# Kernel optimization log

Hardware: AMD Instinct MI355X
Metric: run time of the kernel (lower is better)

Reference implementation:

```python
import jax, jax.numpy as jnp
from jax import lax
import numpy as np

# ---- module hyperparameters (from init_kwargs) ----
DIM = 256
DIM_HEAD = 64
HEADS = 4
GROUPS = 4                      # offset_groups (defaults to heads)
INNER = DIM_HEAD * HEADS        # 256
OFF_DIMS = INNER // GROUPS      # 64
DOWN = 4
KS = 6
PAD = (KS - DOWN) // 2          # 1
OFFSET_SCALE = float(DOWN)      # offset_scale defaults to down_sample_factor
CPB_DIM = DIM // 4              # 64
SCALE = DIM_HEAD ** -0.5


def make_grid(h, w, dtype):
    # torch.meshgrid(arange(w), arange(h), indexing='xy') stacked at dim 0:
    # channel 0 = x (column index), channel 1 = y (row index); shape [2,h,w]
    yy, xx = jnp.meshgrid(jnp.arange(h), jnp.arange(w), indexing='ij')
    return jnp.stack([xx, yy], axis=0).astype(dtype)


def normalize_grid_c(vg):
    # vg: [..., 2, h, w] -> [..., h, w, 2]; faithful to source: channel 0
    # normalized by (h-1), channel 1 by (w-1) (source's h/w naming quirk).
    h, w = vg.shape[-2:]
    gh = 2.0 * vg[..., 0, :, :] / max(h - 1, 1) - 1.0
    gw = 2.0 * vg[..., 1, :, :] / max(w - 1, 1) - 1.0
    return jnp.stack([gh, gw], axis=-1)


def grid_sample_zeros(img, grid):
    # F.grid_sample bilinear, padding_mode='zeros', align_corners=False
    # img: [N,C,H,W]; grid: [N,Hg,Wg,2] with (..,0)=x, (..,1)=y in [-1,1]
    N, C, H, W = img.shape
    ix = ((grid[..., 0] + 1.0) * W - 1.0) * 0.5
    iy = ((grid[..., 1] + 1.0) * H - 1.0) * 0.5
    x0 = jnp.floor(ix)
    y0 = jnp.floor(iy)

    def gather(yy, xx):
        valid = (xx >= 0) & (xx <= W - 1) & (yy >= 0) & (yy <= H - 1)
        xc = jnp.clip(xx, 0, W - 1).astype(jnp.int32)
        yc = jnp.clip(yy, 0, H - 1).astype(jnp.int32)
        vals = jax.vmap(lambda im, y_, x_: im[:, y_, x_])(img, yc, xc)  # [N,C,Hg,Wg]
        return vals * valid[:, None, :, :].astype(img.dtype)

    wa = (x0 + 1 - ix) * (y0 + 1 - iy)
    wb = (ix - x0) * (y0 + 1 - iy)
    wc = (x0 + 1 - ix) * (iy - y0)
    wd = (ix - x0) * (iy - y0)
    return (gather(y0, x0) * wa[:, None]
            + gather(y0, x0 + 1) * wb[:, None]
            + gather(y0 + 1, x0) * wc[:, None]
            + gather(y0 + 1, x0 + 1) * wd[:, None])


def gconv1x1(t, w):
    # grouped 1x1 conv (no bias): t [b, G*Ci, h, w], w [G, Co, Ci]
    G, Co, Ci = w.shape
    bb, _, hh, ww = t.shape
    tg = t.reshape(bb, G, Ci, hh, ww)
    return jnp.einsum('bgihw,goi->bgohw', tg, w).reshape(bb, G * Co, hh, ww)


def setup_inputs() -> dict:
    key = jax.random.key(0)
    ks = jax.random.split(key, 12)
    s = 0.02
    B, H, W = 8, 32, 32
    cg = DIM // GROUPS  # per-group in-channels = 64
    og = INNER // GROUPS  # per-group out-channels = 64
    return {
        'x': jax.random.normal(ks[0], (B, DIM, H, W), jnp.float32),
        'wq': jax.random.normal(ks[1], (GROUPS, og, cg), jnp.float32) * s,
        'wk': jax.random.normal(ks[2], (GROUPS, og, cg), jnp.float32) * s,
        'wv': jax.random.normal(ks[3], (GROUPS, og, cg), jnp.float32) * s,
        'w_off_dw': jax.random.normal(ks[4], (OFF_DIMS, 1, KS, KS), jnp.float32) * s,
        'b_off_dw': jnp.zeros((OFF_DIMS,), jnp.float32),
        'w_off_pw': jax.random.normal(ks[5], (2, OFF_DIMS), jnp.float32) * s,
        'cpb_w1': jax.random.normal(ks[6], (CPB_DIM, 2), jnp.float32) * s,
        'cpb_b1': jnp.zeros((CPB_DIM,), jnp.float32),
        'cpb_w2': jax.random.normal(ks[7], (CPB_DIM, CPB_DIM), jnp.float32) * s,
        'cpb_b2': jnp.zeros((CPB_DIM,), jnp.float32),
        'cpb_w3': jax.random.normal(ks[8], (HEADS // GROUPS, CPB_DIM), jnp.float32) * s,
        'cpb_b3': jnp.zeros((HEADS // GROUPS,), jnp.float32),
        'w_out': jax.random.normal(ks[9], (DIM, INNER), jnp.float32) * s,
        'b_out': jnp.zeros((DIM,), jnp.float32),
    }


def reference(x, wq, wk, wv, w_off_dw, b_off_dw, w_off_pw,
              cpb_w1, cpb_b1, cpb_w2, cpb_b2, cpb_w3, cpb_b3,
              w_out, b_out):
    b, _, H, W = x.shape

    q = gconv1x1(x, wq)                                       # [b, INNER, H, W]
    gq = q.reshape(b * GROUPS, OFF_DIMS, H, W)                # grouped queries
    gx = x.reshape(b * GROUPS, DIM // GROUPS, H, W)           # grouped input

    # to_offsets: depthwise conv -> GELU -> 1x1 conv -> tanh -> scale
    off = lax.conv_general_dilated(
        gq, w_off_dw, window_strides=(DOWN, DOWN),
        padding=[(PAD, PAD), (PAD, PAD)],
        dimension_numbers=('NCHW', 'OIHW', 'NCHW'),
        feature_group_count=OFF_DIMS)
    off = off + b_off_dw[None, :, None, None]
    off = jax.nn.gelu(off, approximate=False)
    off = jnp.einsum('bchw,oc->bohw', off, w_off_pw)
    off = jnp.tanh(off) * OFFSET_SCALE                        # [bg, 2, h2, w2]

    h2, w2 = off.shape[-2:]
    vg = make_grid(h2, w2, off.dtype)[None] + off             # [bg, 2, h2, w2]
    vgs = normalize_grid_c(vg)                                # [bg, h2, w2, 2]

    kv = grid_sample_zeros(gx, vgs)                           # [bg, DIM/G, h2, w2]
    kv = kv.reshape(b, DIM, h2, w2)
    k = gconv1x1(kv, wk)
    v = gconv1x1(kv, wv)
    q = q * SCALE

    def to_heads(t):
        bb, _, hh, ww = t.shape
        return t.reshape(bb, HEADS, DIM_HEAD, hh * ww).transpose(0, 1, 3, 2)

    qh, kh, vh = to_heads(q), to_heads(k), to_heads(v)        # [b, h, i|j, d]
    sim = jnp.einsum('bhid,bhjd->bhij', qh, kh)               # [b, h, HW, h2*w2]

    # CPB relative position bias
    grid_q = normalize_grid_c(make_grid(H, W, x.dtype)).reshape(1, H * W, 2)
    grid_kv = vgs.reshape(b * GROUPS, h2 * w2, 2)
    pos = grid_q[:, :, None, :] - grid_kv[:, None, :, :]      # [bg, i, j, 2]
    bias = jnp.sign(pos) * jnp.log1p(jnp.abs(pos))
    bias = jax.nn.relu(bias @ cpb_w1.T + cpb_b1)
    bias = jax.nn.relu(bias @ cpb_w2.T + cpb_b2)
    bias = bias @ cpb_w3.T + cpb_b3                           # [bg, i, j, o]
    o = HEADS // GROUPS
    bias = bias.reshape(b, GROUPS, H * W, h2 * w2, o)
    bias = bias.transpose(0, 1, 4, 2, 3).reshape(b, HEADS, H * W, h2 * w2)

    attn = jax.nn.softmax(sim + bias, axis=-1)
    out = jnp.einsum('bhij,bhjd->bhid', attn, vh)             # [b, h, HW, d]
    out = out.transpose(0, 1, 3, 2).reshape(b, INNER, H, W)
    out = jnp.einsum('bchw,oc->bohw', out, w_out) + b_out[None, :, None, None]
    return out
```

## Files before the change

kernel.cpp:

```cpp
#include <hip/hip_runtime.h>
#include <hip/hip_bf16.h>
#include <math.h>

#define QSCALE 0.125f

typedef __attribute__((ext_vector_type(8))) short short8b;
typedef __attribute__((ext_vector_type(8))) _Float16 half8;
typedef __attribute__((ext_vector_type(2))) _Float16 half2v;
typedef __attribute__((ext_vector_type(4))) float f32x4;

__device__ __forceinline__ uint pack2(float a, float b) {
    uint r;
    asm("v_cvt_pk_bf16_f32 %0, %1, %2" : "=v"(r) : "v"(a), "v"(b));
    return r;
}
__device__ __forceinline__ uint pkrtz(float a, float b) {
    uint r;
    asm("v_cvt_pkrtz_f16_f32 %0, %1, %2" : "=v"(r) : "v"(a), "v"(b));
    return r;
}
__device__ __forceinline__ half2v h2(uint u) { return __builtin_bit_cast(half2v, u); }
__device__ __forceinline__ float slogf_(float p) {
    return copysignf(log1pf(fabsf(p)), p);
}

__global__ __launch_bounds__(256) void k_qproj(const float* __restrict__ x,
                                               const float* __restrict__ wq,
                                               float* __restrict__ q,
                                               short* __restrict__ qbt) {
    __shared__ float Wst[64 * 68];
    __shared__ float xs[64 * 68];
    int ht = blockIdx.x, g = blockIdx.y, b = blockIdx.z;
    int tid = threadIdx.x;
    for (int e = tid; e < 4096; e += 256) {
        int co = e >> 6, ci = e & 63;
        Wst[ci * 68 + co] = wq[(g * 64 + co) * 64 + ci];
    }
    const float* xb = x + (b * 256 + g * 64) * 1024 + ht * 64;
    for (int e = tid; e < 1024; e += 256) {
        int ci = e >> 4, hq = e & 15;
        *(float4*)&xs[ci * 68 + hq * 4] = *(const float4*)&xb[ci * 1024 + hq * 4];
    }
    __syncthreads();
    int cg = tid >> 4, hg = tid & 15;
    int co0 = cg * 4, hw0 = hg * 4;
    float acc[4][4] = {};
    for (int ci = 0; ci < 64; ci++) {
        float4 a4 = *(float4*)&Wst[ci * 68 + co0];
        float4 b4 = *(float4*)&xs[ci * 68 + hw0];
        float av[4] = {a4.x, a4.y, a4.z, a4.w};
        float bv[4] = {b4.x, b4.y, b4.z, b4.w};
        #pragma unroll
        for (int a = 0; a < 4; a++)
            #pragma unroll
            for (int c = 0; c < 4; c++) acc[a][c] += av[a] * bv[c];
    }
    float* qb = q + (b * 256 + g * 64) * 1024 + ht * 64;
    for (int a = 0; a < 4; a++) {
        float4 o = {acc[a][0], acc[a][1], acc[a][2], acc[a][3]};
        *(float4*)&qb[(co0 + a) * 1024 + hw0] = o;
    }
    short* q16 = qbt + ((size_t)((b * 4 + g) * 1024 + ht * 64)) * 64;
    for (int c = 0; c < 4; c++) {
        uint2 uu;
        uu.x = pack2(acc[0][c] * QSCALE, acc[1][c] * QSCALE);
        uu.y = pack2(acc[2][c] * QSCALE, acc[3][c] * QSCALE);
        *(uint2*)&q16[(hw0 + c) * 64 + co0] = uu;
    }
}

__global__ __launch_bounds__(256) void k_dw(const float* __restrict__ q,
                                            const float* __restrict__ wdw,
                                            const float* __restrict__ bdw,
                                            float* __restrict__ gdw) {
    __shared__ float qs[8 * 1024];
    __shared__ float wds[8 * 36];
    int cg = blockIdx.x, n = blockIdx.y;
    int b = n >> 2, gg = n & 3;
    int c0 = cg * 8;
    int tid = threadIdx.x;
    const float* qn = q + (b * 256 + gg * 64 + c0) * 1024;
    for (int e = tid; e < 2048; e += 256)
        ((float4*)qs)[e] = ((const float4*)qn)[e];
    for (int e = tid; e < 288; e += 256)
        wds[e] = wdw[c0 * 36 + e];
    __syncthreads();
    for (int e = tid; e < 512; e += 256) {
        int c = e >> 6, pos = e & 63;
        int oy = pos >> 3, ox = pos & 7;
        float acc = bdw[c0 + c];
        #pragma unroll
        for (int ky = 0; ky < 6; ky++) {
            int iy = oy * 4 - 1 + ky;
            if (iy < 0 || iy > 31) continue;
            #pragma unroll
            for (int kx = 0; kx < 6; kx++) {
                int ix = ox * 4 - 1 + kx;
                if (ix < 0 || ix > 31) continue;
                acc += qs[c * 1024 + iy * 32 + ix] * wds[c * 36 + ky * 6 + kx];
            }
        }
        gdw[(n * 64 + c0 + c) * 64 + pos] = acc * 0.5f * (1.f + erff(acc * 0.70710678118654752f));
    }
}

__global__ __launch_bounds__(256) void k_pre(const float* __restrict__ x,
                                             const float* __restrict__ gdw,
                                             const float* __restrict__ wpw,
                                             const float* __restrict__ wk,
                                             const float* __restrict__ wv,
                                             const float* __restrict__ wout,
                                             const float* __restrict__ w2,
                                             float* __restrict__ vgs,
                                             uint* __restrict__ u0g,
                                             short* __restrict__ kob,
                                             short* __restrict__ vob,
                                             short* __restrict__ wob,
                                             uint* __restrict__ w2h) {
    __shared__ float gstage[4096];
    __shared__ float kvsT[64 * 68];
    __shared__ uint wkh[64 * 36];
    __shared__ uint wvh[64 * 36];
    __shared__ uint kvh[64 * 36];
    __shared__ float vx_s[64], vy_s[64];
    int n = blockIdx.x, tid = threadIdx.x;
    int b = n >> 2, g = n & 3;

    {
        int e = n * 2048 + tid * 8;
        float4 f0 = *(const float4*)&wout[e];
        float4 f1 = *(const float4*)&wout[e + 4];
        uint4 u = {pack2(f0.x, f0.y), pack2(f0.z, f0.w), pack2(f1.x, f1.y), pack2(f1.z, f1.w)};
        *(uint4*)&wob[e] = u;
    }
    if (tid < 128) {
        int idx = n * 128 + tid;
        int c2 = idx >> 5, p = idx & 31;
        float2 wv2 = *(const float2*)&w2[c2 * 64 + 2 * p];
        w2h[c2 * 32 + p] = pkrtz(wv2.x, wv2.y);
    }
    for (int e = tid; e < 2048; e += 256) {
        int co = e >> 5, p = e & 31;
        float2 a = *(const float2*)&wk[(g * 64 + co) * 64 + 2 * p];
        float2 c = *(const float2*)&wv[(g * 64 + co) * 64 + 2 * p];
        wkh[co * 36 + p] = pkrtz(a.x, a.y);
        wvh[co * 36 + p] = pkrtz(c.x, c.y);
    }
    for (int e = tid; e < 1024; e += 256)
        ((float4*)gstage)[e] = ((const float4*)(gdw + n * 4096))[e];
    __syncthreads();
    if (tid < 128) {
        int o = tid >> 6, pos = tid & 63;
        float a = 0.f;
        #pragma unroll 8
        for (int c = 0; c < 64; c++) a += gstage[c * 64 + pos] * wpw[o * 64 + c];
        float off = tanhf(a) * 4.0f;
        if (o == 0) {
            int ox = pos & 7;
            float v = 2.f * ((float)ox + off) / 7.f - 1.f;
            vx_s[pos] = v;
            vgs[(n * 64 + pos) * 2] = v;
        } else {
            int oy = pos >> 3;
            float v = 2.f * ((float)oy + off) / 7.f - 1.f;
            vy_s[pos] = v;
            vgs[(n * 64 + pos) * 2 + 1] = v;
        }
    }
    __syncthreads();
    for (int e = tid; e < 2048; e += 256) {
        int ix = e >> 6, j = e & 63;
        float qx = (2.f / 31.f) * (float)ix - 1.f;
        float u = slogf_(qx - vx_s[j]);
        u0g[n * 2048 + e] = pkrtz(u, u);
    }
    for (int e = tid; e < 4096; e += 256) {
        int c = e >> 6, pos = e & 63;
        float ix = (vx_s[pos] + 1.f) * 16.f - 0.5f;
        float iy = (vy_s[pos] + 1.f) * 16.f - 0.5f;
        float x0 = floorf(ix), y0 = floorf(iy);
        float wa = (x0 + 1.f - ix) * (y0 + 1.f - iy);
        float wb = (ix - x0) * (y0 + 1.f - iy);
        float wc = (x0 + 1.f - ix) * (iy - y0);
        float wd = (ix - x0) * (iy - y0);
        const float* img = x + (b * 256 + g * 64 + c) * 1024;
        int xi = (int)x0, yi = (int)y0;
        float acc = 0.f;
        if (xi >= 0 && xi <= 31 && yi >= 0 && yi <= 31)             acc += img[yi * 32 + xi] * wa;
        if (xi + 1 >= 0 && xi + 1 <= 31 && yi >= 0 && yi <= 31)     acc += img[yi * 32 + xi + 1] * wb;
        if (xi >= 0 && xi <= 31 && yi + 1 >= 0 && yi + 1 <= 31)     acc += img[(yi + 1) * 32 + xi] * wc;
        if (xi + 1 >= 0 && xi + 1 <= 31 && yi + 1 >= 0 && yi + 1 <= 31) acc += img[(yi + 1) * 32 + xi + 1] * wd;
        kvsT[pos * 68 + c] = acc;
    }
    __syncthreads();
    for (int e = tid; e < 2048; e += 256) {
        int pos = e >> 5, p = e & 31;
        float2 v2 = *(const float2*)&kvsT[pos * 68 + 2 * p];
        kvh[pos * 36 + p] = pkrtz(v2.x, v2.y);
    }
    __syncthreads();
    int wid = tid >> 6, lane = tid & 63, lr = lane & 15, gq = lane >> 4;
    int mat = wid >> 1, cb = (wid & 1) * 32;
    const uint* wh = mat ? wvh : wkh;
    #pragma unroll
    for (int ct2 = 0; ct2 < 2; ct2++) {
        int ct = cb + ct2 * 16;
        half8 af[2];
        #pragma unroll
        for (int s = 0; s < 2; s++)
            af[s] = __builtin_bit_cast(half8, *(const uint4*)&wh[(ct + lr) * 36 + s * 16 + gq * 4]);
        #pragma unroll
        for (int nt = 0; nt < 4; nt++) {
            half8 bf[2];
            #pragma unroll
            for (int s = 0; s < 2; s++)
                bf[s] = __builtin_bit_cast(half8, *(const uint4*)&kvh[(nt * 16 + lr) * 36 + s * 16 + gq * 4]);
            f32x4 acc = {0.f, 0.f, 0.f, 0.f};
            acc = __builtin_amdgcn_mfma_f32_16x16x32_f16(af[0], bf[0], acc, 0, 0, 0);
            acc = __builtin_amdgcn_mfma_f32_16x16x32_f16(af[1], bf[1], acc, 0, 0, 0);
            if (mat == 0) {
                uint2 uu = {pack2(acc[0], acc[1]), pack2(acc[2], acc[3])};
                *(uint2*)&kob[n * 4096 + (nt * 16 + lr) * 64 + ct + gq * 4] = uu;
            } else {
                #pragma unroll
                for (int r = 0; r < 4; r++)
                    vob[n * 4096 + (ct + gq * 4 + r) * 64 + nt * 16 + lr] = (short)pack2(acc[r], acc[r]);
            }
        }
    }
}

__global__ __launch_bounds__(256) void k_cpb(const float* __restrict__ vgs,
                                             const uint* __restrict__ u0g,
                                             const float* __restrict__ w1,
                                             const float* __restrict__ b1,
                                             const uint* __restrict__ w2h,
                                             const float* __restrict__ b2,
                                             const float* __restrict__ w3,
                                             const float* __restrict__ b3,
                                             float* __restrict__ bias) {
    __shared__ uint Q1p[64 * 36];
    __shared__ uint u0p[16 * 64];
    __shared__ float u1t[64];
    __shared__ uint w1ps[32];
    __shared__ float w3s[64];
    __shared__ float b2s[64];
    int iy = blockIdx.x >> 1, xh = blockIdx.x & 1, n = blockIdx.y, tid = threadIdx.x;
    float qy = 2.f * (float)iy / 31.f - 1.f;

    if (tid < 64) u1t[tid] = slogf_(qy - vgs[(n << 7) + tid * 2 + 1]);
    if (tid >= 64 && tid < 96) {
        int p = tid - 64;
        int s = p >> 4, gg = (p >> 2) & 3, pp = p & 3;
        int k = s * 32 + gg * 8 + 2 * pp;
        w1ps[p] = pkrtz(w1[2 * k], w1[2 * k + 2]);
    }
    if (tid >= 128 && tid < 192) w3s[tid - 128] = w3[tid - 128];
    if (tid >= 192) b2s[tid - 192] = b2[tid - 192];
    __syncthreads();
    for (int e = tid; e < 2048; e += 256) {
        int j = e >> 5, pp = e & 31;
        int k = pp * 2;
        float lo = fmaf(w1[2 * k + 1], u1t[j], b1[k]);
        float hi = fmaf(w1[2 * k + 3], u1t[j], b1[k + 1]);
        Q1p[j * 36 + pp] = pkrtz(lo, hi);
    }
    for (int e = tid; e < 1024; e += 256)
        u0p[e] = u0g[n * 2048 + xh * 1024 + e];

    int wid = tid >> 6, lane = tid & 63, lr = lane & 15, g = lane >> 4;
    float b3v = b3[0];

    half8 w2f[4][2];
    #pragma unroll
    for (int m = 0; m < 4; m++)
        #pragma unroll
        for (int s = 0; s < 2; s++)
            w2f[m][s] = __builtin_bit_cast(half8,
                *(const uint4*)&w2h[(m * 16 + lr) * 32 + s * 16 + g * 4]);
    __syncthreads();

    const half2v hz = {(_Float16)0, (_Float16)0};
    for (int ii = 0; ii < 4; ii++) {
        int ixl = wid * 4 + ii;
        int iG = iy * 32 + xh * 16 + ixl;
        float* brow = &bias[((size_t)n * 1024 + iG) * 64];
        #pragma unroll
        for (int nt = 0; nt < 4; nt++) {
            half2v u0v = h2(u0p[ixl * 64 + nt * 16 + lr]);
            const uint* q1p = &Q1p[(nt * 16 + lr) * 36];
            half8 bfr[2];
            #pragma unroll
            for (int s = 0; s < 2; s++) {
                uint4 q4 = *(const uint4*)&q1p[s * 16 + g * 4];
                uint4 wp4 = *(const uint4*)&w1ps[s * 16 + g * 4];
                half2v h0 = __builtin_elementwise_max(h2(wp4.x) * u0v + h2(q4.x), hz);
                half2v h1v = __builtin_elementwise_max(h2(wp4.y) * u0v + h2(q4.y), hz);
                half2v h2v_ = __builtin_elementwise_max(h2(wp4.z) * u0v + h2(q4.z), hz);
                half2v h3 = __builtin_elementwise_max(h2(wp4.w) * u0v + h2(q4.w), hz);
                uint4 hb = {__builtin_bit_cast(uint, h0), __builtin_bit_cast(uint, h1v),
                            __builtin_bit_cast(uint, h2v_), __builtin_bit_cast(uint, h3)};
                bfr[s] = __builtin_bit_cast(half8, hb);
            }
            f32x4 acc[4];
            #pragma unroll
            for (int m = 0; m < 4; m++) {
                f32x4 cseed = *(const f32x4*)&b2s[m * 16 + g * 4];
                acc[m] = __builtin_amdgcn_mfma_f32_16x16x32_f16(w2f[m][0], bfr[0], cseed, 0, 0, 0);
            }
            #pragma unroll
            for (int m = 0; m < 4; m++)
                acc[m] = __builtin_amdgcn_mfma_f32_16x16x32_f16(w2f[m][1], bfr[1], acc[m], 0, 0, 0);
            f32x4 tv = {0.f, 0.f, 0.f, 0.f};
            #pragma unroll
            for (int m = 0; m < 4; m++) {
                f32x4 r = __builtin_elementwise_max(acc[m], (f32x4){0.f, 0.f, 0.f, 0.f});
                f32x4 w3m = *(const f32x4*)&w3s[m * 16 + g * 4];
                tv += w3m * r;
            }
            float t = (tv[0] + tv[1]) + (tv[2] + tv[3]);
            t += __shfl_xor(t, 16);
            t += __shfl_xor(t, 32);
            if (g == nt) brow[lane] = t + b3v;
        }
    }
}

__global__ __launch_bounds__(256) void k_attn(const short* __restrict__ qbt,
                                              const short* __restrict__ kob,
                                              const short* __restrict__ vob,
                                              const float* __restrict__ bias,
                                              short* __restrict__ attb) {
    __shared__ float scr[4][1088];
    int it = blockIdx.x, h = blockIdx.y, b = blockIdx.z;
    int n = b * 4 + h;
    int tid = threadIdx.x, wid = tid >> 6, lane = tid & 63, lr = lane & 15, g = lane >> 4;
    int i0w = it * 64 + wid * 16;
    float* P = scr[wid];

    const short* kb = kob + n * 4096;
    short8b kf[4][2];
    #pragma unroll
    for (int nt = 0; nt < 4; nt++)
        #pragma unroll
        for (int s = 0; s < 2; s++)
            kf[nt][s] = *(const short8b*)&kb[(nt * 16 + lr) * 64 + s * 32 + g * 8];
    const short* vb = vob + n * 4096;
    short8b vf[4][2];
    #pragma unroll
    for (int nt = 0; nt < 4; nt++)
        #pragma unroll
        for (int s = 0; s < 2; s++)
            vf[nt][s] = *(const short8b*)&vb[(nt * 16 + lr) * 64 + s * 32 + g * 8];
    const short* qb = qbt + ((size_t)n * 1024 + i0w + lr) * 64;
    short8b qf[2];
    qf[0] = *(const short8b*)&qb[g * 8];
    qf[1] = *(const short8b*)&qb[32 + g * 8];
    float bv[4][4];
    #pragma unroll
    for (int r = 0; r < 4; r++)
        #pragma unroll
        for (int nt = 0; nt < 4; nt++)
            bv[r][nt] = bias[((size_t)n * 1024 + i0w + g * 4 + r) * 64 + nt * 16 + lr];

    f32x4 acc[4];
    #pragma unroll
    for (int nt = 0; nt < 4; nt++) acc[nt] = (f32x4){0.f, 0.f, 0.f, 0.f};
    #pragma unroll
    for (int s = 0; s < 2; s++)
        #pragma unroll
        for (int nt = 0; nt < 4; nt++)
            acc[nt] = __builtin_amdgcn_mfma_f32_16x16x32_bf16(qf[s], kf[nt][s], acc[nt], 0, 0, 0);

    #pragma unroll
    for (int r = 0; r < 4; r++) {
        float s0 = acc[0][r] + bv[r][0], s1 = acc[1][r] + bv[r][1];
        float s2 = acc[2][r] + bv[r][2], s3 = acc[3][r] + bv[r][3];
        float m = fmaxf(fmaxf(s0, s1), fmaxf(s2, s3));
        m = fmaxf(m, __shfl_xor(m, 1));
        m = fmaxf(m, __shfl_xor(m, 2));
        m = fmaxf(m, __shfl_xor(m, 4));
        m = fmaxf(m, __shfl_xor(m, 8));
        float e0 = __expf(s0 - m), e1 = __expf(s1 - m);
        float e2 = __expf(s2 - m), e3 = __expf(s3 - m);
        float sum = (e0 + e1) + (e2 + e3);
        sum += __shfl_xor(sum, 1);
        sum += __shfl_xor(sum, 2);
        sum += __shfl_xor(sum, 4);
        sum += __shfl_xor(sum, 8);
        float inv = 1.f / sum;
        int row = g * 4 + r;
        P[row * 68 + lr]      = e0 * inv;
        P[row * 68 + 16 + lr] = e1 * inv;
        P[row * 68 + 32 + lr] = e2 * inv;
        P[row * 68 + 48 + lr] = e3 * inv;
    }

    const float* pr = &P[lr * 68];
    float4 a0 = *(float4*)&pr[g * 8];
    float4 a1 = *(float4*)&pr[g * 8 + 4];
    float4 a2 = *(float4*)&pr[32 + g * 8];
    float4 a3 = *(float4*)&pr[32 + g * 8 + 4];
    uint4 up0 = {pack2(a0.x, a0.y), pack2(a0.z, a0.w), pack2(a1.x, a1.y), pack2(a1.z, a1.w)};
    uint4 up1 = {pack2(a2.x, a2.y), pack2(a2.z, a2.w), pack2(a3.x, a3.y), pack2(a3.z, a3.w)};
    short8b pf0 = __builtin_bit_cast(short8b, up0);
    short8b pf1 = __builtin_bit_cast(short8b, up1);

    f32x4 oacc[4];
    #pragma unroll
    for (int nt = 0; nt < 4; nt++) oacc[nt] = (f32x4){0.f, 0.f, 0.f, 0.f};
    #pragma unroll
    for (int nt = 0; nt < 4; nt++) {
        oacc[nt] = __builtin_amdgcn_mfma_f32_16x16x32_bf16(pf0, vf[nt][0], oacc[nt], 0, 0, 0);
        oacc[nt] = __builtin_amdgcn_mfma_f32_16x16x32_bf16(pf1, vf[nt][1], oacc[nt], 0, 0, 0);
    }

    #pragma unroll
    for (int nt = 0; nt < 4; nt++)
        #pragma unroll
        for (int r = 0; r < 4; r++)
            P[(nt * 16 + lr) * 17 + g * 4 + r] = oacc[nt][r];
    int il = lane >> 2, dq = lane & 3;
    uint ub[8];
    #pragma unroll
    for (int t = 0; t < 8; t++) {
        float lo = P[(dq * 16 + 2 * t) * 17 + il];
        float hi = P[(dq * 16 + 2 * t + 1) * 17 + il];
        ub[t] = pack2(lo, hi);
    }
    short* op = attb + ((size_t)(b * 1024 + i0w + il)) * 256 + h * 64 + dq * 16;
    uint4 s0v = {ub[0], ub[1], ub[2], ub[3]};
    uint4 s1v = {ub[4], ub[5], ub[6], ub[7]};
    ((uint4*)op)[0] = s0v;
    ((uint4*)op)[1] = s1v;
}

__global__ __launch_bounds__(256) void k_outproj(const short* __restrict__ attb,
                                                 const short* __restrict__ wob,
                                                 const float* __restrict__ bout,
                                                 float* __restrict__ y) {
    int rt = blockIdx.x;
    int ct = blockIdx.y;
    int tid = threadIdx.x, wid = tid >> 6, lane = tid & 63, lr = lane & 15, g = lane >> 4;
    int wr = wid >> 1, wc = wid & 1;
    int b = rt >> 5;
    int hw0 = (rt & 31) * 32 + wr * 16;
    int cobase = ct * 128 + wc * 64;
    const short* arow = attb + ((size_t)(b * 1024) + hw0) * 256;
    const short* brow = wob + (size_t)cobase * 256;

    f32x4 acc[4];
    #pragma unroll
    for (int nn = 0; nn < 4; nn++) acc[nn] = (f32x4){0.f, 0.f, 0.f, 0.f};
    #pragma unroll
    for (int s = 0; s < 8; s++) {
        short8b af = *(const short8b*)&arow[lr * 256 + s * 32 + g * 8];
        #pragma unroll
        for (int nn = 0; nn < 4; nn++) {
            short8b bf = *(const short8b*)&brow[(nn * 16 + lr) * 256 + s * 32 + g * 8];
            acc[nn] = __builtin_amdgcn_mfma_f32_16x16x32_bf16(af, bf, acc[nn], 0, 0, 0);
        }
    }
    #pragma unroll
    for (int nn = 0; nn < 4; nn++) {
        int co = cobase + nn * 16 + lr;
        float bo = bout[co];
        float4 o = {acc[nn][0] + bo, acc[nn][1] + bo, acc[nn][2] + bo, acc[nn][3] + bo};
        *(float4*)&y[(size_t)b * 262144 + (size_t)co * 1024 + hw0 + g * 4] = o;
    }
}

extern "C" void kernel_launch(void* const* d_in, const int* in_sizes, int n_in,
                              void* d_out, int out_size, void* d_ws, size_t ws_size,
                              hipStream_t stream) {
    const float* x    = (const float*)d_in[0];
    const float* wq   = (const float*)d_in[1];
    const float* wk   = (const float*)d_in[2];
    const float* wv   = (const float*)d_in[3];
    const float* wdw  = (const float*)d_in[4];
    const float* bdw  = (const float*)d_in[5];
    const float* wpw  = (const float*)d_in[6];
    const float* cw1  = (const float*)d_in[7];
    const float* cb1  = (const float*)d_in[8];
    const float* cw2  = (const float*)d_in[9];
    const float* cb2  = (const float*)d_in[10];
    const float* cw3  = (const float*)d_in[11];
    const float* cb3  = (const float*)d_in[12];
    const float* wout = (const float*)d_in[13];
    const float* bout = (const float*)d_in[14];
    float* y  = (float*)d_out;
    float* ws = (float*)d_ws;

    float* q    = ws;
    short* attb = (short*)ws;
    float* bias = ws + 2097152;
    float* vgs  = ws + 4325376;
    short* qbt  = (short*)(ws + 4329472);
    short* kob  = (short*)(ws + 5378048);
    short* vob  = (short*)(ws + 5443584);
    float* gdw  = ws + 5509120;
    short* wob  = (short*)(ws + 5640192);
    uint*  u0g  = (uint*)(ws + 5672960);
    uint*  w2h  = (uint*)(ws + 5738496);

    k_qproj  <<<dim3(16, 4, 8), 256, 0, stream>>>(x, wq, q, qbt);
    k_dw     <<<dim3(8, 32),    256, 0, stream>>>(q, wdw, bdw, gdw);
    k_pre    <<<32,             256, 0, stream>>>(x, gdw, wpw, wk, wv, wout, cw2,
                                                  vgs, u0g, kob, vob, wob, w2h);
    k_cpb    <<<dim3(64, 32),   256, 0, stream>>>(vgs, u0g, cw1, cb1, w2h, cb2, cw3, cb3, bias);
    k_attn   <<<dim3(16, 4, 8), 256, 0, stream>>>(qbt, kob, vob, bias, attb);
    k_outproj<<<dim3(256, 2),   256, 0, stream>>>(attb, wob, bout, y);
}
```

Measured before the change: 100.3 us.

## Fuse attention into CPB bias kernel, keeping bias tile in shared memory

```diff
diff --git a/kernel.cpp b/kernel.cpp
--- a/kernel.cpp
+++ b/kernel.cpp
@@ -238,13 +238,17 @@
                                              const float* __restrict__ b2,
                                              const float* __restrict__ w3,
                                              const float* __restrict__ b3,
-                                             float* __restrict__ bias) {
+                                             const short* __restrict__ qbt,
+                                             const short* __restrict__ kob,
+                                             const short* __restrict__ vob,
+                                             short* __restrict__ attb) {
     __shared__ uint Q1p[64 * 36];
     __shared__ uint u0p[16 * 64];
     __shared__ float u1t[64];
     __shared__ uint w1ps[32];
     __shared__ float w3s[64];
     __shared__ float b2s[64];
+    __shared__ float biasS[16 * 68];
     int iy = blockIdx.x >> 1, xh = blockIdx.x & 1, n = blockIdx.y, tid = threadIdx.x;
     float qy = 2.f * (float)iy / 31.f - 1.f;
 
@@ -283,8 +287,6 @@
     const half2v hz = {(_Float16)0, (_Float16)0};
     for (int ii = 0; ii < 4; ii++) {
         int ixl = wid * 4 + ii;
-        int iG = iy * 32 + xh * 16 + ixl;
-        float* brow = &bias[((size_t)n * 1024 + iG) * 64];
         #pragma unroll
         for (int nt = 0; nt < 4; nt++) {
             half2v u0v = h2(u0p[ixl * 64 + nt * 16 + lr]);
@@ -321,118 +323,98 @@
             float t = (tv[0] + tv[1]) + (tv[2] + tv[3]);
             t += __shfl_xor(t, 16);
             t += __shfl_xor(t, 32);
-            if (g == nt) brow[lane] = t + b3v;
-        }
-    }
-}
-
-__global__ __launch_bounds__(256) void k_attn(const short* __restrict__ qbt,
-                                              const short* __restrict__ kob,
-                                              const short* __restrict__ vob,
-                                              const float* __restrict__ bias,
-                                              short* __restrict__ attb) {
-    __shared__ float scr[4][1088];
-    int it = blockIdx.x, h = blockIdx.y, b = blockIdx.z;
-    int n = b * 4 + h;
-    int tid = threadIdx.x, wid = tid >> 6, lane = tid & 63, lr = lane & 15, g = lane >> 4;
-    int i0w = it * 64 + wid * 16;
-    float* P = scr[wid];
-
-    const short* kb = kob + n * 4096;
-    short8b kf[4][2];
-    #pragma unroll
-    for (int nt = 0; nt < 4; nt++)
-        #pragma unroll
-        for (int s = 0; s < 2; s++)
-            kf[nt][s] = *(const short8b*)&kb[(nt * 16 + lr) * 64 + s * 32 + g * 8];
-    const short* vb = vob + n * 4096;
-    short8b vf[4][2];
-    #pragma unroll
-    for (int nt = 0; nt < 4; nt++)
-        #pragma unroll
-        for (int s = 0; s < 2; s++)
-            vf[nt][s] = *(const short8b*)&vb[(nt * 16 + lr) * 64 + s * 32 + g * 8];
-    const short* qb = qbt + ((size_t)n * 1024 + i0w + lr) * 64;
-    short8b qf[2];
-    qf[0] = *(const short8b*)&qb[g * 8];
-    qf[1] = *(const short8b*)&qb[32 + g * 8];
-    float bv[4][4];
-    #pragma unroll
-    for (int r = 0; r < 4; r++)
+            if (g == nt) biasS[ixl * 68 + lane] = t + b3v;
+        }
+    }
+    __syncthreads();
+
+    if (wid == 0) {
+        float* P = biasS;
+        int i0w = iy * 32 + xh * 16;
+        const short* kb = kob + n * 4096;
+        const short* vb = vob + n * 4096;
+        const short* qb = qbt + ((size_t)n * 1024 + i0w + lr) * 64;
+        short8b qf[2];
+        qf[0] = *(const short8b*)&qb[g * 8];
+        qf[1] = *(const short8b*)&qb[32 + g * 8];
+        float bv[4][4];
+        #pragma unroll
+        for (int r = 0; r < 4; r++)
+            #pragma unroll
+            for (int nt = 0; nt < 4; nt++)
+                bv[r][nt] = biasS[(g * 4 + r) * 68 + nt * 16 + lr];
+
+        f32x4 acc[4];
+        #pragma unroll
+        for (int nt = 0; nt < 4; nt++) {
+            short8b kf0 = *(const short8b*)&kb[(nt * 16 + lr) * 64 + g * 8];
+            short8b kf1 = *(const short8b*)&kb[(nt * 16 + lr) * 64 + 32 + g * 8];
+            acc[nt] = (f32x4){0.f, 0.f, 0.f, 0.f};
+            acc[nt] = __builtin_amdgcn_mfma_f32_16x16x32_bf16(qf[0], kf0, acc[nt], 0, 0, 0);
+            acc[nt] = __builtin_amdgcn_mfma_f32_16x16x32_bf16(qf[1], kf1, acc[nt], 0, 0, 0);
+        }
+        #pragma unroll
+        for (int r = 0; r < 4; r++) {
+            float s0 = acc[0][r] + bv[r][0], s1 = acc[1][r] + bv[r][1];
+            float s2 = acc[2][r] + bv[r][2], s3 = acc[3][r] + bv[r][3];
+            float m = fmaxf(fmaxf(s0, s1), fmaxf(s2, s3));
+            m = fmaxf(m, __shfl_xor(m, 1));
+            m = fmaxf(m, __shfl_xor(m, 2));
+            m = fmaxf(m, __shfl_xor(m, 4));
+            m = fmaxf(m, __shfl_xor(m, 8));
+            float e0 = __expf(s0 - m), e1 = __expf(s1 - m);
+            float e2 = __expf(s2 - m), e3 = __expf(s3 - m);
+            float sum = (e0 + e1) + (e2 + e3);
+            sum += __shfl_xor(sum, 1);
+            sum += __shfl_xor(sum, 2);
+            sum += __shfl_xor(sum, 4);
+            sum += __shfl_xor(sum, 8);
+            float inv = 1.f / sum;
+            int row = g * 4 + r;
+            P[row * 68 + lr]      = e0 * inv;
+            P[row * 68 + 16 + lr] = e1 * inv;
+            P[row * 68 + 32 + lr] = e2 * inv;
+            P[row * 68 + 48 + lr] = e3 * inv;
+        }
+        const float* pr = &P[lr * 68];
+        float4 a0 = *(float4*)&pr[g * 8];
+        float4 a1 = *(float4*)&pr[g * 8 + 4];
+        float4 a2 = *(float4*)&pr[32 + g * 8];
+        float4 a3 = *(float4*)&pr[32 + g * 8 + 4];
+        uint4 up0 = {pack2(a0.x, a0.y), pack2(a0.z, a0.w), pack2(a1.x, a1.y), pack2(a1.z, a1.w)};
+        uint4 up1 = {pack2(a2.x, a2.y), pack2(a2.z, a2.w), pack2(a3.x, a3.y), pack2(a3.z, a3.w)};
+        short8b pf0 = __builtin_bit_cast(short8b, up0);
+        short8b pf1 = __builtin_bit_cast(short8b, up1);
+
+        f32x4 oacc[4];
+        #pragma unroll
+        for (int nt = 0; nt < 4; nt++) {
+            short8b vf0 = *(const short8b*)&vb[(nt * 16 + lr) * 64 + g * 8];
+            short8b vf1 = *(const short8b*)&vb[(nt * 16 + lr) * 64 + 32 + g * 8];
+            oacc[nt] = (f32x4){0.f, 0.f, 0.f, 0.f};
+            oacc[nt] = __builtin_amdgcn_mfma_f32_16x16x32_bf16(pf0, vf0, oacc[nt], 0, 0, 0);
+            oacc[nt] = __builtin_amdgcn_mfma_f32_16x16x32_bf16(pf1, vf1, oacc[nt], 0, 0, 0);
+        }
         #pragma unroll
         for (int nt = 0; nt < 4; nt++)
-            bv[r][nt] = bias[((size_t)n * 1024 + i0w + g * 4 + r) * 64 + nt * 16 + lr];
-
-    f32x4 acc[4];
-    #pragma unroll
-    for (int nt = 0; nt < 4; nt++) acc[nt] = (f32x4){0.f, 0.f, 0.f, 0.f};
-    #pragma unroll
-    for (int s = 0; s < 2; s++)
-        #pragma unroll
-        for (int nt = 0; nt < 4; nt++)
-            acc[nt] = __builtin_amdgcn_mfma_f32_16x16x32_bf16(qf[s], kf[nt][s], acc[nt], 0, 0, 0);
-
-    #pragma unroll
-    for (int r = 0; r < 4; r++) {
-        float s0 = acc[0][r] + bv[r][0], s1 = acc[1][r] + bv[r][1];
-        float s2 = acc[2][r] + bv[r][2], s3 = acc[3][r] + bv[r][3];
-        float m = fmaxf(fmaxf(s0, s1), fmaxf(s2, s3));
-        m = fmaxf(m, __shfl_xor(m, 1));
-        m = fmaxf(m, __shfl_xor(m, 2));
-        m = fmaxf(m, __shfl_xor(m, 4));
-        m = fmaxf(m, __shfl_xor(m, 8));
-        float e0 = __expf(s0 - m), e1 = __expf(s1 - m);
-        float e2 = __expf(s2 - m), e3 = __expf(s3 - m);
-        float sum = (e0 + e1) + (e2 + e3);
-        sum += __shfl_xor(sum, 1);
-        sum += __shfl_xor(sum, 2);
-        sum += __shfl_xor(sum, 4);
-        sum += __shfl_xor(sum, 8);
-        float inv = 1.f / sum;
-        int row = g * 4 + r;
-        P[row * 68 + lr]      = e0 * inv;
-        P[row * 68 + 16 + lr] = e1 * inv;
-        P[row * 68 + 32 + lr] = e2 * inv;
-        P[row * 68 + 48 + lr] = e3 * inv;
-    }
-
-    const float* pr = &P[lr * 68];
-    float4 a0 = *(float4*)&pr[g * 8];
-    float4 a1 = *(float4*)&pr[g * 8 + 4];
-    float4 a2 = *(float4*)&pr[32 + g * 8];
-    float4 a3 = *(float4*)&pr[32 + g * 8 + 4];
-    uint4 up0 = {pack2(a0.x, a0.y), pack2(a0.z, a0.w), pack2(a1.x, a1.y), pack2(a1.z, a1.w)};
-    uint4 up1 = {pack2(a2.x, a2.y), pack2(a2.z, a2.w), pack2(a3.x, a3.y), pack2(a3.z, a3.w)};
-    short8b pf0 = __builtin_bit_cast(short8b, up0);
-    short8b pf1 = __builtin_bit_cast(short8b, up1);
-
-    f32x4 oacc[4];
-    #pragma unroll
-    for (int nt = 0; nt < 4; nt++) oacc[nt] = (f32x4){0.f, 0.f, 0.f, 0.f};
-    #pragma unroll
-    for (int nt = 0; nt < 4; nt++) {
-        oacc[nt] = __builtin_amdgcn_mfma_f32_16x16x32_bf16(pf0, vf[nt][0], oacc[nt], 0, 0, 0);
-        oacc[nt] = __builtin_amdgcn_mfma_f32_16x16x32_bf16(pf1, vf[nt][1], oacc[nt], 0, 0, 0);
-    }
-
-    #pragma unroll
-    for (int nt = 0; nt < 4; nt++)
-        #pragma unroll
-        for (int r = 0; r < 4; r++)
-            P[(nt * 16 + lr) * 17 + g * 4 + r] = oacc[nt][r];
-    int il = lane >> 2, dq = lane & 3;
-    uint ub[8];
-    #pragma unroll
-    for (int t = 0; t < 8; t++) {
-        float lo = P[(dq * 16 + 2 * t) * 17 + il];
-        float hi = P[(dq * 16 + 2 * t + 1) * 17 + il];
-        ub[t] = pack2(lo, hi);
-    }
-    short* op = attb + ((size_t)(b * 1024 + i0w + il)) * 256 + h * 64 + dq * 16;
-    uint4 s0v = {ub[0], ub[1], ub[2], ub[3]};
-    uint4 s1v = {ub[4], ub[5], ub[6], ub[7]};
-    ((uint4*)op)[0] = s0v;
-    ((uint4*)op)[1] = s1v;
+            #pragma unroll
+            for (int r = 0; r < 4; r++)
+                P[(nt * 16 + lr) * 17 + g * 4 + r] = oacc[nt][r];
+        int il = lane >> 2, dq = lane & 3;
+        uint ub[8];
+        #pragma unroll
+        for (int t = 0; t < 8; t++) {
+            float lo = P[(dq * 16 + 2 * t) * 17 + il];
+            float hi = P[(dq * 16 + 2 * t + 1) * 17 + il];
+            ub[t] = pack2(lo, hi);
+        }
+        int b_ = n >> 2, h_ = n & 3;
+        short* op = attb + ((size_t)(b_ * 1024 + i0w + il)) * 256 + h_ * 64 + dq * 16;
+        uint4 s0v = {ub[0], ub[1], ub[2], ub[3]};
+        uint4 s1v = {ub[4], ub[5], ub[6], ub[7]};
+        ((uint4*)op)[0] = s0v;
+        ((uint4*)op)[1] = s1v;
+    }
 }
 
 __global__ __launch_bounds__(256) void k_outproj(const short* __restrict__ attb,
@@ -493,7 +475,6 @@
 
     float* q    = ws;
     short* attb = (short*)ws;
-    float* bias = ws + 2097152;
     float* vgs  = ws + 4325376;
     short* qbt  = (short*)(ws + 4329472);
     short* kob  = (short*)(ws + 5378048);
@@ -507,7 +488,7 @@
     k_dw     <<<dim3(8, 32),    256, 0, stream>>>(q, wdw, bdw, gdw);
     k_pre    <<<32,             256, 0, stream>>>(x, gdw, wpw, wk, wv, wout, cw2,
                                                   vgs, u0g, kob, vob, wob, w2h);
-    k_cpb    <<<dim3(64, 32),   256, 0, stream>>>(vgs, u0g, cw1, cb1, w2h, cb2, cw3, cb3, bias);
-    k_attn   <<<dim3(16, 4, 8), 256, 0, stream>>>(qbt, kob, vob, bias, attb);
+    k_cpb    <<<dim3(64, 32),   256, 0, stream>>>(vgs, u0g, cw1, cb1, w2h, cb2, cw3, cb3,
+                                                  qbt, kob, vob, attb);
     k_outproj<<<dim3(256, 2),   256, 0, stream>>>(attb, wob, bout, y);
 }
```

New measurement: 100.4 us. No clear change (+0.1%).
